# Kernel optimization log

Measured on AMD Instinct MI355X. Metric: run time of the kernel, lower is better.

The kernel has to match this reference:

```python
import jax, jax.numpy as jnp
import numpy as np

B, T, D, H = 2, 2048, 1024, 16
HD = D // H
ALPHA = HD ** -0.5
EPS = 1e-5


def setup_inputs() -> dict:
    key = jax.random.key(0)
    ks = jax.random.split(key, 8)
    x = jax.random.normal(ks[0], (B, T, D), dtype=jnp.float32)
    # additive causal mask: 0 where allowed, -inf where disallowed
    causal = jnp.triu(jnp.ones((T, T), dtype=bool), k=1)
    attention_mask = jnp.where(causal, -jnp.inf, 0.0).astype(jnp.float32)
    rab = jax.random.normal(ks[1], (1, H, T, T), dtype=jnp.float32) * 0.02
    W_in = jax.random.normal(ks[2], (D, 4 * D), dtype=jnp.float32) * (D ** -0.5)
    b_in = jnp.zeros((4 * D,), dtype=jnp.float32)
    W_out = jax.random.normal(ks[3], (D, D), dtype=jnp.float32) * (D ** -0.5)
    b_out = jnp.zeros((D,), dtype=jnp.float32)
    ln_w = jnp.ones((D,), dtype=jnp.float32)
    ln_b = jnp.zeros((D,), dtype=jnp.float32)
    return {"x": x, "attention_mask": attention_mask, "rab": rab,
            "W_in": W_in, "b_in": b_in, "W_out": W_out, "b_out": b_out,
            "ln_w": ln_w, "ln_b": ln_b}


def _heads(t):  # [B,T,D] -> [B,H,T,HD]
    return t.reshape(B, T, H, HD).transpose(0, 2, 1, 3)


def _layernorm(t, w, b):
    mu = jnp.mean(t, axis=-1, keepdims=True)
    var = jnp.mean(jnp.square(t - mu), axis=-1, keepdims=True)
    return (t - mu) * jax.lax.rsqrt(var + EPS) * w + b


def reference(x, attention_mask, rab, W_in, b_in, W_out, b_out, ln_w, ln_b):
    h = jax.nn.silu(x @ W_in + b_in)                      # [B,T,4D]
    U, V, Q, K = jnp.split(h, 4, axis=-1)
    Qh, Kh, Vh = _heads(Q), _heads(K), _heads(V)
    logits = jnp.einsum('bhqd,bhkd->bhqk', Qh, Kh) * ALPHA
    logits = logits + rab + attention_mask[None, None]    # [B,H,T,T]
    # allowed counts from the additive mask (0 == allowed)
    allowed = (attention_mask == 0).astype(jnp.float32)   # [T,T]
    denom = jnp.clip(jnp.sum(allowed, axis=-1, keepdims=True), 1.0)  # [T,1]
    logits_safe = jnp.where(jnp.isinf(logits) & (logits < 0), -1e9, logits)
    attn = jax.nn.silu(logits_safe) / denom[None, None]
    AV = jnp.einsum('bhqk,bhkd->bhqd', attn, Vh)
    AV = AV.transpose(0, 2, 1, 3).reshape(B, T, D)
    y = (_layernorm(AV, ln_w, ln_b) * U) @ W_out + b_out
    return y
```

## Files before the change

kernel.cpp:

```cpp
#include <hip/hip_runtime.h>

#define BATCH 2
#define TSEQ 2048
#define DIM 1024
#define NH 16
#define HDIM 64
#define MROWS (BATCH * TSEQ)

typedef __attribute__((ext_vector_type(4))) float f32x4;
typedef __attribute__((ext_vector_type(8))) short short8;

__device__ __forceinline__ unsigned short f2bf(float f) {
    union { float f; unsigned int u; } x; x.f = f;
    unsigned int r = x.u + 0x7fffu + ((x.u >> 16) & 1u);
    return (unsigned short)(r >> 16);
}

__device__ __forceinline__ float bf2f(unsigned short s) {
    union { unsigned int u; float f; } t; t.u = (unsigned int)s << 16;
    return t.f;
}

__device__ __forceinline__ float silu_f(float v) {
    return v * __builtin_amdgcn_rcpf(1.f + __expf(-v));
}

__device__ __forceinline__ void gl_lds16(const void* g, void* l) {
    __builtin_amdgcn_global_load_lds(
        (const __attribute__((address_space(1))) void*)g,
        (__attribute__((address_space(3))) void*)l, 16, 0, 0);
}

__device__ __forceinline__ short8 rd_swz(const unsigned short* base, int row, int chunk) {
    const char* b = (const char*)base;
    return *(const short8*)(b + row * 128 + (((chunk ^ (row & 7)) << 4)));
}

__global__ __launch_bounds__(256) void k_convert(const float* __restrict__ in,
                                                 unsigned short* __restrict__ out,
                                                 int n4) {
    int i = blockIdx.x * 256 + threadIdx.x;
    if (i < n4) {
        float4 v = ((const float4*)in)[i];
        union { unsigned short s[4]; uint2 u; } o;
        o.s[0] = f2bf(v.x); o.s[1] = f2bf(v.y); o.s[2] = f2bf(v.z); o.s[3] = f2bf(v.w);
        ((uint2*)out)[i] = o.u;
    }
}

__global__ __launch_bounds__(256) void k_transpose(const float* __restrict__ in,
                                                   unsigned short* __restrict__ out,
                                                   int R, int C) {
    __shared__ float tile[32][33];
    int tx = threadIdx.x, ty = threadIdx.y;
    int c0 = blockIdx.x * 32, r0 = blockIdx.y * 32;
    #pragma unroll
    for (int i = 0; i < 32; i += 8)
        tile[ty + i][tx] = in[(size_t)(r0 + ty + i) * C + c0 + tx];
    __syncthreads();
    #pragma unroll
    for (int i = 0; i < 32; i += 8)
        out[(size_t)(c0 + ty + i) * R + r0 + tx] = f2bf(tile[tx][ty + i]);
}

__device__ __forceinline__ void stage256(const unsigned short* __restrict__ A,
                                         const unsigned short* __restrict__ Bt,
                                         int row0, int col0, int k0,
                                         unsigned short* sAbuf, unsigned short* sBbuf,
                                         int tid) {
    #pragma unroll
    for (int q = 0; q < 4; ++q) {
        int c = tid + 512 * q;
        int rr = c >> 3;
        int kcs = (c & 7) ^ (rr & 7);
        gl_lds16(A + (size_t)(row0 + rr) * 1024 + k0 + kcs * 8, sAbuf + c * 8);
        gl_lds16(Bt + (size_t)(col0 + rr) * 1024 + k0 + kcs * 8, sBbuf + c * 8);
    }
}

__global__ __launch_bounds__(512, 2) void k_gemm1_256(
    const unsigned short* __restrict__ A, const unsigned short* __restrict__ Bt,
    const float* __restrict__ bias,
    unsigned short* __restrict__ outU, unsigned short* __restrict__ outVt,
    unsigned short* __restrict__ outQ, unsigned short* __restrict__ outK)
{
    __shared__ __align__(16) unsigned short sA[2][256 * 64];
    __shared__ __align__(16) unsigned short sB[2][256 * 64];

    const int tid = threadIdx.x;
    const int lane = tid & 63, wid = tid >> 6;
    const int lr = lane & 15, lk = lane >> 4;
    const int wm = wid >> 2, wn = wid & 3;
    const int bm = blockIdx.x, bn = blockIdx.y;
    const int row0 = bm * 256, col0 = bn * 256;

    f32x4 acc[8][4] = {};

    stage256(A, Bt, row0, col0, 0, sA[0], sB[0], tid);
    asm volatile("s_waitcnt vmcnt(0)" ::: "memory");
    __builtin_amdgcn_s_barrier();
    __builtin_amdgcn_sched_barrier(0);

    int cur = 0;
    for (int kt = 0; kt < 16; ++kt) {
        if (kt < 15) stage256(A, Bt, row0, col0, (kt + 1) * 64, sA[cur ^ 1], sB[cur ^ 1], tid);
        short8 bf[2][4];
        #pragma unroll
        for (int kk = 0; kk < 2; ++kk)
            #pragma unroll
            for (int n = 0; n < 4; ++n)
                bf[kk][n] = rd_swz(sB[cur], wn * 64 + n * 16 + lr, kk * 4 + lk);

        #pragma unroll
        for (int ph = 0; ph < 4; ++ph) {
            short8 af[2][2];
            #pragma unroll
            for (int mm = 0; mm < 2; ++mm)
                #pragma unroll
                for (int kk = 0; kk < 2; ++kk)
                    af[mm][kk] = rd_swz(sA[cur], wm * 128 + (ph * 2 + mm) * 16 + lr, kk * 4 + lk);
            __builtin_amdgcn_s_barrier();
            __builtin_amdgcn_s_setprio(1);
            #pragma unroll
            for (int mm = 0; mm < 2; ++mm)
                #pragma unroll
                for (int n = 0; n < 4; ++n)
                    #pragma unroll
                    for (int kk = 0; kk < 2; ++kk)
                        acc[ph * 2 + mm][n] = __builtin_amdgcn_mfma_f32_16x16x32_bf16(
                            af[mm][kk], bf[kk][n], acc[ph * 2 + mm][n], 0, 0, 0);
            __builtin_amdgcn_s_setprio(0);
            if (ph == 3) asm volatile("s_waitcnt vmcnt(0)" ::: "memory");
            __builtin_amdgcn_s_barrier();
        }
        __builtin_amdgcn_sched_barrier(0);
        cur ^= 1;
    }

    const int sec = bn >> 2;
    #pragma unroll
    for (int n = 0; n < 4; ++n) {
        const int cg = col0 + wn * 64 + n * 16 + lr;
        const int cc = cg & 1023;
        const float bv = bias[cg];
        #pragma unroll
        for (int m = 0; m < 8; ++m) {
            const int rg0 = row0 + wm * 128 + m * 16 + lk * 4;
            float sv[4];
            #pragma unroll
            for (int j = 0; j < 4; ++j)
                sv[j] = silu_f(acc[m][n][j] + bv);
            if (sec == 0) {
                #pragma unroll
                for (int j = 0; j < 4; ++j)
                    outU[((size_t)(rg0 + j) << 10) + cc] = f2bf(sv[j]);
            } else if (sec == 1) {
                union { unsigned short s[4]; uint2 u; } pk;
                #pragma unroll
                for (int j = 0; j < 4; ++j) pk.s[j] = f2bf(sv[j]);
                *(uint2*)(outVt + ((size_t)cc << 12) + rg0) = pk.u;
            } else if (sec == 2) {
                #pragma unroll
                for (int j = 0; j < 4; ++j)
                    outQ[((size_t)(rg0 + j) << 10) + cc] = f2bf(sv[j] * 0.125f);
            } else {
                #pragma unroll
                for (int j = 0; j < 4; ++j)
                    outK[((size_t)(rg0 + j) << 10) + cc] = f2bf(sv[j]);
            }
        }
    }
}

__device__ __forceinline__ void stage128(const unsigned short* __restrict__ A,
                                         const unsigned short* __restrict__ Bt,
                                         int row0, int col0, int k0,
                                         unsigned short* sAbuf, unsigned short* sBbuf,
                                         int tid) {
    #pragma unroll
    for (int q = 0; q < 4; ++q) {
        int c = tid + 256 * q;
        int rr = c >> 3;
        int kcs = (c & 7) ^ (rr & 7);
        gl_lds16(A + (size_t)(row0 + rr) * 1024 + k0 + kcs * 8, sAbuf + c * 8);
        gl_lds16(Bt + (size_t)(col0 + rr) * 1024 + k0 + kcs * 8, sBbuf + c * 8);
    }
}

__global__ __launch_bounds__(256, 2) void k_gemm2(
    const unsigned short* __restrict__ A, const unsigned short* __restrict__ Bt,
    const float* __restrict__ bias, float* __restrict__ outY)
{
    __shared__ __align__(16) unsigned short sA[2][128 * 64];
    __shared__ __align__(16) unsigned short sB[2][128 * 64];

    const int tid = threadIdx.x;
    const int lane = tid & 63, wid = tid >> 6;
    const int lr = lane & 15, lk = lane >> 4;
    const int wm = wid >> 1, wn = wid & 1;
    const int bm = blockIdx.x, bn = blockIdx.y;
    const int row0 = bm * 128, col0 = bn * 128;

    f32x4 acc[4][4] = {};

    stage128(A, Bt, row0, col0, 0, sA[0], sB[0], tid);
    asm volatile("s_waitcnt vmcnt(0)" ::: "memory");
    __builtin_amdgcn_s_barrier();
    __builtin_amdgcn_sched_barrier(0);

    int cur = 0;
    for (int kt = 0; kt < 16; ++kt) {
        if (kt < 15) stage128(A, Bt, row0, col0, (kt + 1) * 64, sA[cur ^ 1], sB[cur ^ 1], tid);
        short8 bf[2][4];
        #pragma unroll
        for (int kk = 0; kk < 2; ++kk)
            #pragma unroll
            for (int n = 0; n < 4; ++n)
                bf[kk][n] = rd_swz(sB[cur], wn * 64 + n * 16 + lr, kk * 4 + lk);

        #pragma unroll
        for (int ph = 0; ph < 2; ++ph) {
            short8 af[2][2];
            #pragma unroll
            for (int mm = 0; mm < 2; ++mm)
                #pragma unroll
                for (int kk = 0; kk < 2; ++kk)
                    af[mm][kk] = rd_swz(sA[cur], wm * 64 + (ph * 2 + mm) * 16 + lr, kk * 4 + lk);
            __builtin_amdgcn_s_barrier();
            __builtin_amdgcn_s_setprio(1);
            #pragma unroll
            for (int mm = 0; mm < 2; ++mm)
                #pragma unroll
                for (int n = 0; n < 4; ++n)
                    #pragma unroll
                    for (int kk = 0; kk < 2; ++kk)
                        acc[ph * 2 + mm][n] = __builtin_amdgcn_mfma_f32_16x16x32_bf16(
                            af[mm][kk], bf[kk][n], acc[ph * 2 + mm][n], 0, 0, 0);
            __builtin_amdgcn_s_setprio(0);
            if (ph == 1) asm volatile("s_waitcnt vmcnt(0)" ::: "memory");
            __builtin_amdgcn_s_barrier();
        }
        __builtin_amdgcn_sched_barrier(0);
        cur ^= 1;
    }

    #pragma unroll
    for (int n = 0; n < 4; ++n) {
        const int cg = col0 + wn * 64 + n * 16 + lr;
        const float bv = bias[cg];
        #pragma unroll
        for (int m = 0; m < 4; ++m) {
            const int rg0 = row0 + wm * 64 + m * 16 + lk * 4;
            #pragma unroll
            for (int j = 0; j < 4; ++j)
                outY[(size_t)(rg0 + j) * 1024 + cg] = acc[m][n][j] + bv;
        }
    }
}

__global__ __launch_bounds__(256, 4) void k_attn(
    const unsigned short* __restrict__ Qb,
    const unsigned short* __restrict__ Kb,
    const unsigned short* __restrict__ Vt,
    const float* __restrict__ rab,
    unsigned short* __restrict__ AV)
{
    __shared__ __align__(16) unsigned short sK[2][64 * 64];
    __shared__ __align__(16) unsigned short sVt[2][64 * 64];
    __shared__ __align__(16) unsigned short sP[64 * 64];

    const int tid = threadIdx.x;
    const int lane = tid & 63;
    const int w = tid >> 6;
    const int lr = lane & 15;
    const int lk = lane >> 4;

    const int bid = blockIdx.x;
    const int idx = bid & 255;
    const int g = bid >> 8;
    const int h = idx & 15;
    const int r_ = idx >> 4;
    const int bb = g >> 1;
    const int qt = (g & 1) ? (31 - r_) : r_;
    const int q0 = qt * 64;

    short8 qreg[2];
    #pragma unroll
    for (int ks = 0; ks < 2; ++ks)
        qreg[ks] = *(const short8*)(Qb + (((size_t)(bb * TSEQ + q0 + w * 16 + lr)) << 10)
                                     + h * 64 + ks * 32 + lk * 8);
    __builtin_amdgcn_sched_barrier(0);

    int qrow[4];
    const float* rabrow[4];
    const float* rabh = rab + (size_t)h * TSEQ * TSEQ;
    #pragma unroll
    for (int j = 0; j < 4; ++j) {
        qrow[j] = q0 + w * 16 + lk * 4 + j;
        rabrow[j] = rabh + (size_t)qrow[j] * TSEQ + lr;
    }

    f32x4 acc[4] = {};

    #define STAGE(buf, kt_) do {                                                      \
        int k0s = (kt_) * 64;                                                         \
        for (int c = tid; c < 512; c += 256) {                                        \
            int rr = c >> 3, kc = c & 7;                                              \
            int kcs = kc ^ (rr & 7);                                                  \
            gl_lds16(Kb + (((size_t)(bb * TSEQ + k0s + rr)) << 10) + h * 64 + kcs * 8,\
                     sK[buf] + c * 8);                                                \
            gl_lds16(Vt + (((size_t)(h * 64 + rr)) << 12) + bb * TSEQ + k0s + kcs * 8,\
                     sVt[buf] + c * 8);                                               \
        }                                                                             \
    } while (0)

    float rv0[4][4], rv1[4][4];

    STAGE(0, 0);
    __builtin_amdgcn_sched_barrier(0);
    #pragma unroll
    for (int nt = 0; nt < 4; ++nt)
        #pragma unroll
        for (int j = 0; j < 4; ++j)
            rv0[nt][j] = rabrow[j][nt * 16];
    __builtin_amdgcn_sched_barrier(0);
    asm volatile("s_waitcnt vmcnt(16)" ::: "memory");
    __builtin_amdgcn_s_barrier();

    #define BODY(KT, BUFC, RVC, RVN) do {                                             \
        const int k0 = (KT) * 64;                                                     \
        const bool have_next = (KT) < qt;                                             \
        if (have_next) STAGE((BUFC) ^ 1, (KT) + 1);                                   \
        __builtin_amdgcn_sched_barrier(0);                                            \
        if (have_next) {                                                              \
            _Pragma("unroll")                                                         \
            for (int nt = 0; nt < 4; ++nt)                                            \
                _Pragma("unroll")                                                     \
                for (int j = 0; j < 4; ++j)                                           \
                    RVN[nt][j] = rabrow[j][k0 + 64 + nt * 16];                        \
        }                                                                             \
        __builtin_amdgcn_sched_barrier(0);                                            \
        f32x4 s[4];                                                                   \
        _Pragma("unroll")                                                             \
        for (int nt = 0; nt < 4; ++nt) {                                              \
            f32x4 c0v;                                                                \
            c0v[0] = RVC[nt][0]; c0v[1] = RVC[nt][1];                                 \
            c0v[2] = RVC[nt][2]; c0v[3] = RVC[nt][3];                                 \
            s[nt] = c0v;                                                              \
        }                                                                             \
        _Pragma("unroll")                                                             \
        for (int ks = 0; ks < 2; ++ks) {                                              \
            _Pragma("unroll")                                                         \
            for (int nt = 0; nt < 4; ++nt)                                            \
                s[nt] = __builtin_amdgcn_mfma_f32_16x16x32_bf16(                      \
                    qreg[ks], rd_swz(sK[BUFC], nt * 16 + lr, ks * 4 + lk), s[nt], 0, 0, 0); \
        }                                                                             \
        char* pb = (char*)sP;                                                         \
        if (have_next) {                                                              \
            _Pragma("unroll")                                                         \
            for (int j = 0; j < 4; ++j) {                                             \
                const int prow = w * 16 + lk * 4 + j;                                 \
                char* bj = pb + prow * 128;                                           \
                const int swz = ((lk * 4 + j) & 7) << 4;                              \
                _Pragma("unroll")                                                     \
                for (int nt = 0; nt < 4; ++nt)                                        \
                    *(unsigned short*)(bj + (((nt << 5) | (lr << 1)) ^ swz))          \
                        = f2bf(silu_f(s[nt][j]));                                     \
            }                                                                         \
        } else {                                                                      \
            _Pragma("unroll")                                                         \
            for (int j = 0; j < 4; ++j) {                                             \
                const int prow = w * 16 + lk * 4 + j;                                 \
                char* bj = pb + prow * 128;                                           \
                const int swz = ((lk * 4 + j) & 7) << 4;                              \
                _Pragma("unroll")                                                     \
                for (int nt = 0; nt < 4; ++nt) {                                      \
                    int k = k0 + nt * 16 + lr;                                        \
                    float pv = (k <= qrow[j]) ? silu_f(s[nt][j]) : 0.f;               \
                    *(unsigned short*)(bj + (((nt << 5) | (lr << 1)) ^ swz)) = f2bf(pv); \
                }                                                                     \
            }                                                                         \
        }                                                                             \
        _Pragma("unroll")                                                             \
        for (int ks = 0; ks < 2; ++ks) {                                              \
            short8 ap = rd_swz(sP, w * 16 + lr, ks * 4 + lk);                         \
            _Pragma("unroll")                                                         \
            for (int dt = 0; dt < 4; ++dt)                                            \
                acc[dt] = __builtin_amdgcn_mfma_f32_16x16x32_bf16(                    \
                    ap, rd_swz(sVt[BUFC], dt * 16 + lr, ks * 4 + lk), acc[dt], 0, 0, 0); \
        }                                                                             \
        if (have_next) {                                                              \
            asm volatile("s_waitcnt vmcnt(16)" ::: "memory");                         \
            __builtin_amdgcn_s_barrier();                                             \
        }                                                                             \
    } while (0)

    for (int kt = 0; kt <= qt; kt += 2) {
        BODY(kt, 0, rv0, rv1);
        if (kt + 1 <= qt) BODY(kt + 1, 1, rv1, rv0);
    }
    #undef BODY
    #undef STAGE

    #pragma unroll
    for (int dt = 0; dt < 4; ++dt)
        #pragma unroll
        for (int j = 0; j < 4; ++j)
            AV[(((size_t)(bb * TSEQ + qrow[j])) << 10) + h * 64 + dt * 16 + lr]
                = f2bf(acc[dt][j]);
}

__global__ __launch_bounds__(256) void k_ln(const unsigned short* __restrict__ AV,
                                            const unsigned short* __restrict__ U,
                                            const float* __restrict__ lnw,
                                            const float* __restrict__ lnb,
                                            unsigned short* __restrict__ z) {
    __shared__ float red[8];
    const int row = blockIdx.x, tid = threadIdx.x;
    const float c = (float)((row & (TSEQ - 1)) + 1);
    const float eps = 1e-5f * c * c;
    union { unsigned short s[4]; uint2 u; } a;
    a.u = ((const uint2*)(AV + ((size_t)row << 10)))[tid];
    float v[4];
    #pragma unroll
    for (int i = 0; i < 4; ++i) v[i] = bf2f(a.s[i]);
    float s = v[0] + v[1] + v[2] + v[3];
    float s2 = v[0] * v[0] + v[1] * v[1] + v[2] * v[2] + v[3] * v[3];
    #pragma unroll
    for (int o = 32; o > 0; o >>= 1) { s += __shfl_xor(s, o); s2 += __shfl_xor(s2, o); }
    const int w = tid >> 6;
    if ((tid & 63) == 0) { red[w] = s; red[4 + w] = s2; }
    __syncthreads();
    s = red[0] + red[1] + red[2] + red[3];
    s2 = red[4] + red[5] + red[6] + red[7];
    const float mu = s * (1.f / 1024.f);
    const float var = s2 * (1.f / 1024.f) - mu * mu;
    const float rstd = rsqrtf(var + eps);
    union { unsigned short s[4]; uint2 u; } uu;
    uu.u = ((const uint2*)(U + ((size_t)row << 10)))[tid];
    float4 lw = ((const float4*)lnw)[tid];
    float4 lb = ((const float4*)lnb)[tid];
    union { unsigned short o[4]; uint2 u; } ov;
    ov.o[0] = f2bf(((v[0] - mu) * rstd * lw.x + lb.x) * bf2f(uu.s[0]));
    ov.o[1] = f2bf(((v[1] - mu) * rstd * lw.y + lb.y) * bf2f(uu.s[1]));
    ov.o[2] = f2bf(((v[2] - mu) * rstd * lw.z + lb.z) * bf2f(uu.s[2]));
    ov.o[3] = f2bf(((v[3] - mu) * rstd * lw.w + lb.w) * bf2f(uu.s[3]));
    ((uint2*)z)[((size_t)row << 8) + tid] = ov.u;
}

extern "C" void kernel_launch(void* const* d_in, const int* in_sizes, int n_in,
                              void* d_out, int out_size, void* d_ws, size_t ws_size,
                              hipStream_t stream) {
    const float* x     = (const float*)d_in[0];
    const float* rab   = (const float*)d_in[2];
    const float* W_in  = (const float*)d_in[3];
    const float* b_in  = (const float*)d_in[4];
    const float* W_out = (const float*)d_in[5];
    const float* b_out = (const float*)d_in[6];
    const float* ln_w  = (const float*)d_in[7];
    const float* ln_b  = (const float*)d_in[8];
    float* y = (float*)d_out;

    char* ws = (char*)d_ws;
    size_t off = 0;
    auto alloc = [&](size_t bytes) -> void* {
        void* p = ws + off;
        off += (bytes + 255) & ~(size_t)255;
        return p;
    };
    unsigned short* WinT  = (unsigned short*)alloc((size_t)4096 * 1024 * 2);
    unsigned short* WoutT = (unsigned short*)alloc((size_t)1024 * 1024 * 2);
    unsigned short* xb    = (unsigned short*)alloc((size_t)MROWS * DIM * 2);
    unsigned short* Ubuf  = (unsigned short*)alloc((size_t)MROWS * DIM * 2);
    unsigned short* Qb    = (unsigned short*)alloc((size_t)MROWS * DIM * 2);
    unsigned short* Kb    = (unsigned short*)alloc((size_t)MROWS * DIM * 2);
    unsigned short* Vtb   = (unsigned short*)alloc((size_t)DIM * MROWS * 2);
    unsigned short* AV    = (unsigned short*)alloc((size_t)MROWS * DIM * 2);
    unsigned short* z     = (unsigned short*)alloc((size_t)MROWS * DIM * 2);

    k_convert<<<dim3(4096), dim3(256), 0, stream>>>(x, xb, MROWS * DIM / 4);
    k_transpose<<<dim3(128, 32), dim3(32, 8), 0, stream>>>(W_in, WinT, 1024, 4096);
    k_transpose<<<dim3(32, 32), dim3(32, 8), 0, stream>>>(W_out, WoutT, 1024, 1024);
    k_gemm1_256<<<dim3(16, 16), dim3(512), 0, stream>>>(xb, WinT, b_in, Ubuf, Vtb, Qb, Kb);
    k_attn<<<dim3(1024), dim3(256), 0, stream>>>(Qb, Kb, Vtb, rab, AV);
    k_ln<<<dim3(MROWS), dim3(256), 0, stream>>>(AV, Ubuf, ln_w, ln_b, z);
    k_gemm2<<<dim3(32, 8), dim3(256), 0, stream>>>(z, WoutT, b_out, y);
}
```

Before: 158.1 us.

## Transpose QK^T MFMA operands so rab loads and P stores vectorize

Swaps the A/B operands of the QK^T MFMA so each lane owns four consecutive key columns of one query row. This lets the relative-bias tile be fetched with float4 loads instead of scalar strided loads, and lets the P tile be written to LDS as packed bf16 pairs in 8-byte stores. It also adjusts the vmcnt wait count to match the fewer load instructions and adds s_setprio around the MFMA sections. The causal-mask logic and the LDS swizzle are reworked for the new lane mapping, so a wrong index would silently corrupt results.

Measured after the change: 156.6 us. Within noise of the previous version (-0.9%).

```diff
diff --git a/kernel.cpp b/kernel.cpp
--- a/kernel.cpp
+++ b/kernel.cpp
@@ -1,4 +1,5 @@
 #include <hip/hip_runtime.h>
+#include <hip/hip_bf16.h>
 
 #define BATCH 2
 #define TSEQ 2048
@@ -23,6 +24,12 @@
 
 __device__ __forceinline__ float silu_f(float v) {
     return v * __builtin_amdgcn_rcpf(1.f + __expf(-v));
+}
+
+__device__ __forceinline__ unsigned int pack_bf16(float lo, float hi) {
+    union { __hip_bfloat162 h; unsigned int u; } r;
+    r.h = __float22bfloat162_rn(float2{lo, hi});
+    return r.u;
 }
 
 __device__ __forceinline__ void gl_lds16(const void* g, void* l) {
@@ -291,14 +298,9 @@
                                      + h * 64 + ks * 32 + lk * 8);
     __builtin_amdgcn_sched_barrier(0);
 
-    int qrow[4];
-    const float* rabrow[4];
-    const float* rabh = rab + (size_t)h * TSEQ * TSEQ;
-    #pragma unroll
-    for (int j = 0; j < 4; ++j) {
-        qrow[j] = q0 + w * 16 + lk * 4 + j;
-        rabrow[j] = rabh + (size_t)qrow[j] * TSEQ + lr;
-    }
+    const int qloc = w * 16 + lr;
+    const int qcol = q0 + qloc;
+    const float* rabq = rab + ((size_t)h * TSEQ + qcol) * TSEQ + lk * 4;
 
     f32x4 acc[4] = {};
 
@@ -314,17 +316,15 @@
         }                                                                             \
     } while (0)
 
-    float rv0[4][4], rv1[4][4];
+    float4 rv0[4], rv1[4];
 
     STAGE(0, 0);
     __builtin_amdgcn_sched_barrier(0);
     #pragma unroll
     for (int nt = 0; nt < 4; ++nt)
-        #pragma unroll
-        for (int j = 0; j < 4; ++j)
-            rv0[nt][j] = rabrow[j][nt * 16];
+        rv0[nt] = *(const float4*)(rabq + nt * 16);
     __builtin_amdgcn_sched_barrier(0);
-    asm volatile("s_waitcnt vmcnt(16)" ::: "memory");
+    asm volatile("s_waitcnt vmcnt(4)" ::: "memory");
     __builtin_amdgcn_s_barrier();
 
     #define BODY(KT, BUFC, RVC, RVN) do {                                             \
@@ -335,62 +335,60 @@
         if (have_next) {                                                              \
             _Pragma("unroll")                                                         \
             for (int nt = 0; nt < 4; ++nt)                                            \
-                _Pragma("unroll")                                                     \
-                for (int j = 0; j < 4; ++j)                                           \
-                    RVN[nt][j] = rabrow[j][k0 + 64 + nt * 16];                        \
+                RVN[nt] = *(const float4*)(rabq + k0 + 64 + nt * 16);                 \
         }                                                                             \
         __builtin_amdgcn_sched_barrier(0);                                            \
         f32x4 s[4];                                                                   \
         _Pragma("unroll")                                                             \
         for (int nt = 0; nt < 4; ++nt) {                                              \
-            f32x4 c0v;                                                                \
-            c0v[0] = RVC[nt][0]; c0v[1] = RVC[nt][1];                                 \
-            c0v[2] = RVC[nt][2]; c0v[3] = RVC[nt][3];                                 \
-            s[nt] = c0v;                                                              \
-        }                                                                             \
+            s[nt][0] = RVC[nt].x; s[nt][1] = RVC[nt].y;                               \
+            s[nt][2] = RVC[nt].z; s[nt][3] = RVC[nt].w;                               \
+        }                                                                             \
+        __builtin_amdgcn_s_setprio(1);                                                \
         _Pragma("unroll")                                                             \
         for (int ks = 0; ks < 2; ++ks) {                                              \
             _Pragma("unroll")                                                         \
             for (int nt = 0; nt < 4; ++nt)                                            \
                 s[nt] = __builtin_amdgcn_mfma_f32_16x16x32_bf16(                      \
-                    qreg[ks], rd_swz(sK[BUFC], nt * 16 + lr, ks * 4 + lk), s[nt], 0, 0, 0); \
-        }                                                                             \
+                    rd_swz(sK[BUFC], nt * 16 + lr, ks * 4 + lk), qreg[ks], s[nt], 0, 0, 0); \
+        }                                                                             \
+        __builtin_amdgcn_s_setprio(0);                                                \
         char* pb = (char*)sP;                                                         \
+        char* paddr = pb + qloc * 128 + ((lk & 1) * 8);                               \
         if (have_next) {                                                              \
             _Pragma("unroll")                                                         \
-            for (int j = 0; j < 4; ++j) {                                             \
-                const int prow = w * 16 + lk * 4 + j;                                 \
-                char* bj = pb + prow * 128;                                           \
-                const int swz = ((lk * 4 + j) & 7) << 4;                              \
-                _Pragma("unroll")                                                     \
-                for (int nt = 0; nt < 4; ++nt)                                        \
-                    *(unsigned short*)(bj + (((nt << 5) | (lr << 1)) ^ swz))          \
-                        = f2bf(silu_f(s[nt][j]));                                     \
+            for (int nt = 0; nt < 4; ++nt) {                                          \
+                unsigned int p01 = pack_bf16(silu_f(s[nt][0]), silu_f(s[nt][1]));     \
+                unsigned int p23 = pack_bf16(silu_f(s[nt][2]), silu_f(s[nt][3]));     \
+                const int chunk = nt * 2 + (lk >> 1);                                 \
+                *(uint2*)(paddr + ((chunk ^ (qloc & 7)) << 4)) = make_uint2(p01, p23);\
             }                                                                         \
         } else {                                                                      \
             _Pragma("unroll")                                                         \
-            for (int j = 0; j < 4; ++j) {                                             \
-                const int prow = w * 16 + lk * 4 + j;                                 \
-                char* bj = pb + prow * 128;                                           \
-                const int swz = ((lk * 4 + j) & 7) << 4;                              \
-                _Pragma("unroll")                                                     \
-                for (int nt = 0; nt < 4; ++nt) {                                      \
-                    int k = k0 + nt * 16 + lr;                                        \
-                    float pv = (k <= qrow[j]) ? silu_f(s[nt][j]) : 0.f;               \
-                    *(unsigned short*)(bj + (((nt << 5) | (lr << 1)) ^ swz)) = f2bf(pv); \
-                }                                                                     \
+            for (int nt = 0; nt < 4; ++nt) {                                          \
+                const int kb = k0 + nt * 16 + lk * 4;                                 \
+                float a0 = (kb + 0 <= qcol) ? silu_f(s[nt][0]) : 0.f;                 \
+                float a1 = (kb + 1 <= qcol) ? silu_f(s[nt][1]) : 0.f;                 \
+                float a2 = (kb + 2 <= qcol) ? silu_f(s[nt][2]) : 0.f;                 \
+                float a3 = (kb + 3 <= qcol) ? silu_f(s[nt][3]) : 0.f;                 \
+                unsigned int p01 = pack_bf16(a0, a1);                                 \
+                unsigned int p23 = pack_bf16(a2, a3);                                 \
+                const int chunk = nt * 2 + (lk >> 1);                                 \
+                *(uint2*)(paddr + ((chunk ^ (qloc & 7)) << 4)) = make_uint2(p01, p23);\
             }                                                                         \
         }                                                                             \
+        __builtin_amdgcn_s_setprio(1);                                                \
         _Pragma("unroll")                                                             \
         for (int ks = 0; ks < 2; ++ks) {                                              \
-            short8 ap = rd_swz(sP, w * 16 + lr, ks * 4 + lk);                         \
+            short8 ap = rd_swz(sP, qloc, ks * 4 + lk);                                \
             _Pragma("unroll")                                                         \
             for (int dt = 0; dt < 4; ++dt)                                            \
                 acc[dt] = __builtin_amdgcn_mfma_f32_16x16x32_bf16(                    \
                     ap, rd_swz(sVt[BUFC], dt * 16 + lr, ks * 4 + lk), acc[dt], 0, 0, 0); \
         }                                                                             \
+        __builtin_amdgcn_s_setprio(0);                                                \
         if (have_next) {                                                              \
-            asm volatile("s_waitcnt vmcnt(16)" ::: "memory");                         \
+            asm volatile("s_waitcnt vmcnt(4)" ::: "memory");                          \
             __builtin_amdgcn_s_barrier();                                             \
         }                                                                             \
     } while (0)
@@ -406,8 +404,8 @@
     for (int dt = 0; dt < 4; ++dt)
         #pragma unroll
         for (int j = 0; j < 4; ++j)
-            AV[(((size_t)(bb * TSEQ + qrow[j])) << 10) + h * 64 + dt * 16 + lr]
-                = f2bf(acc[dt][j]);
+            AV[(((size_t)(bb * TSEQ + q0 + w * 16 + lk * 4 + j)) << 10)
+               + h * 64 + dt * 16 + lr] = f2bf(acc[dt][j]);
 }
 
 __global__ __launch_bounds__(256) void k_ln(const unsigned short* __restrict__ AV,
```
